# Kernel tuning notes

Hardware: AMD Instinct MI355X
Metric: run time of the kernel (lower is better)

The kernel has to match this reference:

```python
import jax, jax.numpy as jnp
import numpy as np

# Dimensions (see shape_source)
B, C, H, W = 8, 3, 256, 256
WIDTH = 32   # FNO width
MODES = 12   # modes1 == modes2
L = 4        # number of FNO layers
GAP = 4      # encoder_de sample_gap
PAD = 9      # trans_net.padding


def _downsample(x):
    # Faithful vectorized form of encoder_de.output: keep indices i % GAP == 0
    # (output size int((N-1)/GAP)+1 == number of multiples of GAP below N).
    return x[:, :, ::GAP, ::GAP]


def _spectral_conv(x, w1, w2):
    # SpectralConv2d: rfft2 -> low-mode complex channel mix -> irfft2
    Hp, Wp = x.shape[-2], x.shape[-1]
    x_ft = jnp.fft.rfft2(x)  # [B, WIDTH, Hp, Wp//2+1] complex64
    out_ft = jnp.zeros((x.shape[0], w1.shape[1], Hp, Wp // 2 + 1), dtype=jnp.complex64)
    out_ft = out_ft.at[:, :, :MODES, :MODES].set(
        jnp.einsum('bixy,ioxy->boxy', x_ft[:, :, :MODES, :MODES], w1))
    out_ft = out_ft.at[:, :, -MODES:, :MODES].set(
        jnp.einsum('bixy,ioxy->boxy', x_ft[:, :, -MODES:, :MODES], w2))
    return jnp.fft.irfft2(out_ft, s=(Hp, Wp))


def _forward(x_en, fc0_w, fc0_b, w1r, w1i, w2r, w2i, pw_w, pw_b,
             fc1_w, fc1_b, fc2_w, fc2_b):
    x_de = _downsample(x_en)
    # fc0 on channels-last, back to channels-first
    x = jnp.einsum('bchw,cd->bdhw', x_en, fc0_w) + fc0_b[None, :, None, None]
    # F.pad(x, [0, PAD, 0, PAD]) pads right/bottom of last two dims
    x = jnp.pad(x, ((0, 0), (0, 0), (0, PAD), (0, PAD)))
    for l in range(L):
        w1 = (w1r[l] + 1j * w1i[l]).astype(jnp.complex64)
        w2 = (w2r[l] + 1j * w2i[l]).astype(jnp.complex64)
        x1 = _spectral_conv(x, w1, w2)
        x2 = jnp.einsum('bihw,oi->bohw', x, pw_w[l]) + pw_b[l][None, :, None, None]
        x = x1 + x2
        if l < L - 1:  # last layer has no activation
            x = jax.nn.gelu(x, approximate=False)  # torch F.gelu default = exact erf
    trans_out = x[..., :-PAD, :-PAD].transpose(0, 2, 3, 1)  # [B,H,W,WIDTH]
    h = jax.nn.gelu(trans_out @ fc1_w + fc1_b, approximate=False)  # [B,H,W,128]
    pred_delta = (h @ fc2_w + fc2_b).transpose(0, 3, 1, 2)          # [B,3,H,W]
    pred = pred_delta + x_en
    pred_de = _downsample(pred)
    return pred_de, x_de, pred, x_en


def setup_inputs() -> dict:
    key = jax.random.key(0)
    ks = jax.random.split(key, 14)
    scale = 1.0 / (WIDTH * WIDTH)
    f32 = jnp.float32
    x_en = jax.random.normal(ks[0], (B, C, H, W), f32)
    ctr = jnp.zeros((B, 1), f32)  # accepted but unused by trans_net.forward
    fc0_w = jax.random.normal(ks[1], (3, WIDTH), f32) * 0.2
    fc0_b = jnp.zeros((WIDTH,), f32)
    # torch.rand(..., dtype=cfloat): uniform [0,1) real and imag parts
    w1r = scale * jax.random.uniform(ks[2], (L, WIDTH, WIDTH, MODES, MODES), f32)
    w1i = scale * jax.random.uniform(ks[3], (L, WIDTH, WIDTH, MODES, MODES), f32)
    w2r = scale * jax.random.uniform(ks[4], (L, WIDTH, WIDTH, MODES, MODES), f32)
    w2i = scale * jax.random.uniform(ks[5], (L, WIDTH, WIDTH, MODES, MODES), f32)
    pw_w = jax.random.normal(ks[6], (L, WIDTH, WIDTH), f32) / np.sqrt(WIDTH)  # 1x1 conv [out,in]
    pw_b = jnp.zeros((L, WIDTH), f32)
    fc1_w = jax.random.normal(ks[7], (WIDTH, 128), f32) / np.sqrt(WIDTH)
    fc1_b = jnp.zeros((128,), f32)
    fc2_w = jax.random.normal(ks[8], (128, 3), f32) / np.sqrt(128.0)
    fc2_b = jnp.zeros((3,), f32)
    return dict(x_en=x_en, ctr=ctr, fc0_w=fc0_w, fc0_b=fc0_b,
                w1r=w1r, w1i=w1i, w2r=w2r, w2i=w2i,
                pw_w=pw_w, pw_b=pw_b, fc1_w=fc1_w, fc1_b=fc1_b,
                fc2_w=fc2_w, fc2_b=fc2_b)


def reference(x_en, ctr, fc0_w, fc0_b, w1r, w1i, w2r, w2i, pw_w, pw_b,
              fc1_w, fc1_b, fc2_w, fc2_b):
    del ctr  # unused in the original trans_net.forward
    return _forward(x_en, fc0_w, fc0_b, w1r, w1i, w2r, w2i, pw_w, pw_b,
                    fc1_w, fc1_b, fc2_w, fc2_b)
```

## Files before the change

kernel.cpp:

```cpp
#include <hip/hip_runtime.h>
#include <math.h>

#define HP 265
#define NPIX 70225
#define ROWF 8480
#define TWO_PI 6.28318530717958647692f

#define OFF_X     0
#define OFF_U     8988800
#define OFF_G     10752640
#define OFF_A     11047552
#define OFF_TFB   12132992
#define OFF_TS    12137600
#define OFF_W1B   12141952
#define OFF_W2B   12144000
#define OFF_PWB   12145024

typedef __attribute__((ext_vector_type(8))) short short8;
typedef __attribute__((ext_vector_type(4))) float f32x4;

__device__ __forceinline__ float gelu_f(float v){
  float x2 = v*v;
  float p  = fmaf(x2, 0.10295597f, 2.30212056f);
  float tn = -v*p;
  float e  = __builtin_amdgcn_exp2f(tn);
  float r  = __builtin_amdgcn_rcpf(1.0f + e);
  return v * r;
}
__device__ __forceinline__ unsigned short f2b(float f){
  unsigned u = __float_as_uint(f);
  u += 0x7FFFu + ((u >> 16) & 1u);
  return (unsigned short)(u >> 16);
}
__device__ __forceinline__ unsigned pk(unsigned short lo, unsigned short hi){
  return (unsigned)lo | ((unsigned)hi << 16);
}

__global__ void k_init(unsigned short* __restrict__ Tfb, unsigned short* __restrict__ Ts,
                       unsigned short* __restrict__ w1b, unsigned short* __restrict__ w2b,
                       unsigned short* __restrict__ pwb,
                       const float* __restrict__ fc1w, const float* __restrict__ fc2w,
                       const float* __restrict__ pw_w){
  int idx = blockIdx.x*256 + threadIdx.x;
  if (idx < 32*288){
    int m = idx / 288, hc = idx % 288;
    unsigned short v = 0;
    if (m < 26 && hc < 265){
      int k = m >> 1;
      int t = (hc*k) % HP;
      float s, c; sincosf(TWO_PI*(float)t/(float)HP, &s, &c);
      v = f2b((m & 1) ? -s : c);
    }
    Tfb[idx] = v;
  }
  if (idx < 272*32){
    int w = idx >> 5, kap = idx & 31;
    unsigned short v = 0;
    if (w < HP && kap < 24){
      int k = kap >> 1;
      int t = (w*k) % HP;
      float s, c; sincosf(TWO_PI*(float)t/(float)HP, &s, &c);
      const float invN = 1.f/70225.f;
      float val = (!(kap&1)) ? invN*(k==0 ? 1.f : 2.f*c)
                             : ((k==0) ? 0.f : -invN*2.f*s);
      v = f2b(val);
    }
    Ts[idx] = v;
  }
  if (idx < 4096){
    int n = idx >> 5, k = idx & 31;
    w1b[idx] = f2b(fc1w[k*128 + n]);
  }
  if (idx < 2048){
    int n = idx >> 7, k = idx & 127;
    w2b[idx] = (n < 3) ? f2b(fc2w[k*3 + n]) : (unsigned short)0;
  }
  if (idx < 4096)
    pwb[idx] = f2b(pw_w[idx]);
}

__global__ __launch_bounds__(256) void k_fc0(const float* __restrict__ xen,
                                             const float* __restrict__ w0,
                                             const float* __restrict__ b0,
                                             unsigned short* __restrict__ xb,
                                             float* __restrict__ out){
  int idx = blockIdx.x*256 + threadIdx.x;
  if (idx >= 8*NPIX) return;
  int w = idx % HP; int t = idx / HP; int h = t % HP; int b = t / HP;
  unsigned short o16[32];
  if (h < 256 && w < 256){
    const float* xp = xen + (((size_t)b*3)*256 + h)*256 + w;
    float c0 = xp[0], c1 = xp[65536], c2 = xp[131072];
    #pragma unroll
    for (int d = 0; d < 32; ++d)
      o16[d] = f2b(b0[d] + c0*w0[d] + c1*w0[32+d] + c2*w0[64+d]);
    size_t be = ((size_t)b*3)*65536 + (h<<8) + w;
    out[1769472 + be]          = c0;
    out[1769472 + be + 65536]  = c1;
    out[1769472 + be + 131072] = c2;
    if (((h|w)&3) == 0){
      size_t db = ((size_t)b*3)*4096 + ((h>>2)<<6) + (w>>2);
      out[98304 + db]        = c0;
      out[98304 + db + 4096] = c1;
      out[98304 + db + 8192] = c2;
    }
  } else {
    #pragma unroll
    for (int d = 0; d < 32; ++d) o16[d] = 0;
  }
  uint4* dst = (uint4*)(xb + (size_t)idx*32);
  #pragma unroll
  for (int q = 0; q < 4; ++q)
    dst[q] = make_uint4(pk(o16[8*q],o16[8*q+1]), pk(o16[8*q+2],o16[8*q+3]),
                        pk(o16[8*q+4],o16[8*q+5]), pk(o16[8*q+6],o16[8*q+7]));
}

__global__ __launch_bounds__(256) void k_dftm(const unsigned short* __restrict__ xb,
                                              const unsigned short* __restrict__ Tfb,
                                              float* __restrict__ U32){
  int tid = threadIdx.x;
  int wv = tid>>6, lane = tid&63, lr = lane&15, g = lane>>4, lk = g*8;
  int n0 = blockIdx.x*64;
  int b  = blockIdx.y;
  int n  = n0 + wv*16 + lr;
  const unsigned short* xcol = xb + (size_t)b*HP*ROWF + n;
  f32x4 acc0 = {0.f,0.f,0.f,0.f}, acc1 = {0.f,0.f,0.f,0.f};
  #pragma unroll
  for (int kc = 0; kc < 9; ++kc){
    short8 hv;
    int hb = kc*32 + lk;
    #pragma unroll
    for (int q = 0; q < 8; ++q){
      int h = hb + q;
      hv[q] = (h < HP) ? (short)xcol[(size_t)h*ROWF] : (short)0;
    }
    short8 aT0 = *(const short8*)&Tfb[lr*288 + kc*32 + lk];
    short8 aT1 = *(const short8*)&Tfb[(16+lr)*288 + kc*32 + lk];
    acc0 = __builtin_amdgcn_mfma_f32_16x16x32_bf16(aT0, hv, acc0, 0,0,0);
    acc1 = __builtin_amdgcn_mfma_f32_16x16x32_bf16(aT1, hv, acc1, 0,0,0);
  }
  if (n < 8480){
    #pragma unroll
    for (int r = 0; r < 4; ++r){
      int m0 = g*4 + r;
      U32[((size_t)b*26 + m0)*8480 + n] = acc0[r];
      int m1 = 16 + m0;
      if (m1 < 26) U32[((size_t)b*26 + m1)*8480 + n] = acc1[r];
    }
  }
}

__global__ __launch_bounds__(256) void k_spec(const float* __restrict__ U32,
                                              const float* __restrict__ w1r,
                                              const float* __restrict__ w1i,
                                              const float* __restrict__ w2r,
                                              const float* __restrict__ w2i,
                                              float2* __restrict__ G, int l){
  __shared__ float part[256*25];
  __shared__ float Xs[32*25];
  int j = blockIdx.x;
  int b = blockIdx.y;
  int ws = blockIdx.z;
  int tid = threadIdx.x;
  int wsub = tid >> 5, i = tid & 31;
  int kk   = (j < 12) ? j : (24 - j);
  bool cj  = (j >= 12);
  float xr[12], xi[12];
  #pragma unroll
  for (int k = 0; k < 12; ++k){ xr[k] = 0.f; xi[k] = 0.f; }
  const float* ubr = U32 + ((size_t)(b*26 + 2*kk))*8480;
  for (int w = ws*8 + wsub; w < HP; w += 16){
    int n = w*32 + i;
    float ux = ubr[n];
    float uy = ubr[8480 + n];
    if (cj) uy = -uy;
    float bs, bc; sincosf(-TWO_PI*(float)w/(float)HP, &bs, &bc);
    float pr = 1.f, pi = 0.f;
    #pragma unroll
    for (int k = 0; k < 12; ++k){
      xr[k] = fmaf(ux, pr, fmaf(-uy, pi, xr[k]));
      xi[k] = fmaf(ux, pi, fmaf( uy, pr, xi[k]));
      float npr = pr*bc - pi*bs;
      pi = fmaf(pr, bs, pi*bc);
      pr = npr;
    }
  }
  #pragma unroll
  for (int k = 0; k < 12; ++k){
    part[tid*25 + 2*k]     = xr[k];
    part[tid*25 + 2*k + 1] = xi[k];
  }
  __syncthreads();
  {
    int sg = tid >> 5;
    int ii = tid & 31;
    #pragma unroll
    for (int s0 = 0; s0 < 3; ++s0){
      int s = sg*3 + s0;
      float acc = 0.f;
      #pragma unroll
      for (int wq = 0; wq < 8; ++wq) acc += part[(wq*32 + ii)*25 + s];
      Xs[ii*25 + s] = acc;
    }
  }
  __syncthreads();
  int ky = (j < 12) ? j : (j - 12);
  const float* wr = (j < 12) ? w1r : w2r;
  const float* wi = (j < 12) ? w1i : w2i;
  float2* Gp = G + (size_t)ws*73728;
  for (int p = tid; p < 384; p += 256){
    int o = p / 12, kx = p % 12;
    size_t wbase = (size_t)l*147456 + (size_t)o*144 + (size_t)ky*12 + kx;
    float gr = 0.f, gi = 0.f;
    #pragma unroll 4
    for (int i2 = 0; i2 < 32; ++i2){
      float xvr = Xs[i2*25 + 2*kx];
      float xvi = Xs[i2*25 + 2*kx + 1];
      float a = wr[wbase + (size_t)i2*4608];
      float c = wi[wbase + (size_t)i2*4608];
      gr += xvr*a - xvi*c;
      gi += xvr*c + xvi*a;
    }
    Gp[((size_t)(b*32 + o)*24 + j)*12 + kx] = make_float2(gr, gi);
  }
}

__global__ __launch_bounds__(320) void k_idft_h(const float2* __restrict__ G,
                                                unsigned short* __restrict__ A16){
  __shared__ float2 gs[288];
  int bo = blockIdx.x;
  for (int i = threadIdx.x; i < 288; i += 320){
    float2 g0 = G[(size_t)bo*288 + i];
    float2 g1 = G[73728 + (size_t)bo*288 + i];
    gs[i] = make_float2(g0.x + g1.x, g0.y + g1.y);
  }
  __syncthreads();
  int h = threadIdx.x;
  if (h >= HP) return;
  float ar[12], ai[12];
  #pragma unroll
  for (int k = 0; k < 12; ++k){ ar[k] = 0.f; ai[k] = 0.f; }
  for (int j = 0; j < 24; ++j){
    int ky = (j < 12) ? j : (241 + j);
    int t = (ky*h) % HP;
    float s, c; sincosf(TWO_PI*(float)t/(float)HP, &s, &c);
    #pragma unroll
    for (int k = 0; k < 12; ++k){
      float2 g = gs[j*12 + k];
      ar[k] = fmaf(g.x, c, fmaf(-g.y, s, ar[k]));
      ai[k] = fmaf(g.x, s, fmaf( g.y, c, ai[k]));
    }
  }
  int b = bo >> 5, o = bo & 31;
  unsigned short o16[32];
  #pragma unroll
  for (int k = 0; k < 12; ++k){ o16[2*k] = f2b(ar[k]); o16[2*k+1] = f2b(ai[k]); }
  #pragma unroll
  for (int k = 24; k < 32; ++k) o16[k] = 0;
  uint4* ap = (uint4*)(A16 + (((size_t)(b*HP + h))*32 + o)*32);
  #pragma unroll
  for (int q = 0; q < 4; ++q)
    ap[q] = make_uint4(pk(o16[8*q],o16[8*q+1]), pk(o16[8*q+2],o16[8*q+3]),
                       pk(o16[8*q+4],o16[8*q+5]), pk(o16[8*q+6],o16[8*q+7]));
}

__global__ __launch_bounds__(256) void k_final(const unsigned short* __restrict__ A16,
                                               const unsigned short* __restrict__ Tsyn,
                                               const unsigned short* __restrict__ pwb,
                                               const float* __restrict__ pw_b,
                                               unsigned short* __restrict__ xb, int l){
  int tid = threadIdx.x;
  int wv = tid>>6, lane = tid&63, lr = lane&15, g = lane>>4, lk = g*8;
  int h = blockIdx.x*4 + wv;
  int b = blockIdx.y;
  if (h >= HP) return;
  const unsigned short* arow = A16 + (size_t)(b*HP + h)*1024;
  short8 aA0 = *(const short8*)&arow[lr*32 + lk];
  short8 aA1 = *(const short8*)&arow[(16+lr)*32 + lk];
  short8 aP0 = *(const short8*)&pwb[l*1024 + lr*32 + lk];
  short8 aP1 = *(const short8*)&pwb[l*1024 + (16+lr)*32 + lk];
  float4 vb0 = *(const float4*)&pw_b[l*32 + g*4];
  float4 vb1 = *(const float4*)&pw_b[l*32 + 16 + g*4];
  unsigned short* xrow = xb + (size_t)(b*HP + h)*ROWF;
  const f32x4 z4 = {0.f,0.f,0.f,0.f};
  for (int wt = 0; wt < 17; ++wt){
    int w = wt*16 + lr;
    short8 bT = *(const short8*)&Tsyn[(size_t)w*32 + lk];
    short8 bX = *(const short8*)&xrow[(size_t)w*32 + lk];
    f32x4 a0 = __builtin_amdgcn_mfma_f32_16x16x32_bf16(aA0, bT, z4, 0,0,0);
    a0 = __builtin_amdgcn_mfma_f32_16x16x32_bf16(aP0, bX, a0, 0,0,0);
    f32x4 a1 = __builtin_amdgcn_mfma_f32_16x16x32_bf16(aA1, bT, z4, 0,0,0);
    a1 = __builtin_amdgcn_mfma_f32_16x16x32_bf16(aP1, bX, a1, 0,0,0);
    if (w < HP){
      float v0[4], v1[4];
      v0[0]=a0[0]+vb0.x; v0[1]=a0[1]+vb0.y; v0[2]=a0[2]+vb0.z; v0[3]=a0[3]+vb0.w;
      v1[0]=a1[0]+vb1.x; v1[1]=a1[1]+vb1.y; v1[2]=a1[2]+vb1.z; v1[3]=a1[3]+vb1.w;
      if (l < 3){
        #pragma unroll
        for (int r = 0; r < 4; ++r){ v0[r] = gelu_f(v0[r]); v1[r] = gelu_f(v1[r]); }
      }
      *(uint2*)&xrow[(size_t)w*32 + g*4] =
          make_uint2(pk(f2b(v0[0]),f2b(v0[1])), pk(f2b(v0[2]),f2b(v0[3])));
      *(uint2*)&xrow[(size_t)w*32 + 16 + g*4] =
          make_uint2(pk(f2b(v1[0]),f2b(v1[1])), pk(f2b(v1[2]),f2b(v1[3])));
    }
  }
}

__global__ __launch_bounds__(256) void k_head(const unsigned short* __restrict__ xb,
                                              const float* __restrict__ xen,
                                              const unsigned short* __restrict__ w1b,
                                              const float* __restrict__ fc1b,
                                              const unsigned short* __restrict__ w2b,
                                              const float* __restrict__ fc2b,
                                              float* __restrict__ out){
  __shared__ unsigned short Pm[4][16*136];
  int tid = threadIdx.x;
  int b = blockIdx.x >> 8, h = blockIdx.x & 255;
  int wv = tid>>6, lane = tid&63, lr = lane&15, g = lane>>4, lk = g*8;
  short8 bf1[8], bf2[4];
  #pragma unroll
  for (int nt = 0; nt < 8; ++nt)
    bf1[nt] = *(const short8*)&w1b[(nt*16+lr)*32 + lk];
  #pragma unroll
  for (int ks = 0; ks < 4; ++ks)
    bf2[ks] = *(const short8*)&w2b[lr*128 + ks*32 + lk];
  float f2c = (lr < 3) ? fc2b[lr] : 0.f;
  const unsigned short* xrow = xb + (size_t)(b*HP + h)*ROWF;
  unsigned short* P = Pm[wv];
  const f32x4 z4 = {0.f,0.f,0.f,0.f};
  #pragma unroll
  for (int m = 0; m < 4; ++m){
    int p0 = (wv*4 + m)*16;
    short8 ax = *(const short8*)&xrow[(size_t)(p0 + lr)*32 + lk];
    f32x4 acc[8];
    #pragma unroll
    for (int nt = 0; nt < 8; ++nt)
      acc[nt] = __builtin_amdgcn_mfma_f32_16x16x32_bf16(bf1[nt], ax, z4, 0,0,0);
    #pragma unroll
    for (int nt = 0; nt < 8; ++nt){
      float4 bb = *(const float4*)&fc1b[nt*16 + g*4];
      float h0 = gelu_f(acc[nt][0] + bb.x);
      float h1 = gelu_f(acc[nt][1] + bb.y);
      float h2 = gelu_f(acc[nt][2] + bb.z);
      float h3 = gelu_f(acc[nt][3] + bb.w);
      *(uint2*)&P[lr*136 + nt*16 + g*4] =
          make_uint2(pk(f2b(h0),f2b(h1)), pk(f2b(h2),f2b(h3)));
    }
    asm volatile("s_waitcnt lgkmcnt(0)" ::: "memory");
    __builtin_amdgcn_sched_barrier(0);
    f32x4 a2 = z4;
    #pragma unroll
    for (int ks = 0; ks < 4; ++ks){
      short8 ap = *(const short8*)&P[lr*136 + ks*32 + lk];
      a2 = __builtin_amdgcn_mfma_f32_16x16x32_bf16(ap, bf2[ks], a2, 0,0,0);
    }
    if (lr < 3){
      size_t base = ((size_t)(b*3 + lr))*65536 + (h<<8) + p0 + g*4;
      float4 xe = *(const float4*)&xen[base];
      float4 pr;
      pr.x = a2[0] + f2c + xe.x;
      pr.y = a2[1] + f2c + xe.y;
      pr.z = a2[2] + f2c + xe.z;
      pr.w = a2[3] + f2c + xe.w;
      *(float4*)&out[196608 + base] = pr;
      if ((h & 3) == 0){
        int w4 = (p0 + g*4) >> 2;
        out[((size_t)(b*3 + lr))*4096 + ((h>>2)<<6) + w4] = pr.x;
      }
    }
  }
}

extern "C" void kernel_launch(void* const* d_in, const int* in_sizes, int n_in,
                              void* d_out, int out_size, void* d_ws, size_t ws_size,
                              hipStream_t stream){
  const float* x_en  = (const float*)d_in[0];
  const float* fc0_w = (const float*)d_in[2];
  const float* fc0_b = (const float*)d_in[3];
  const float* w1r   = (const float*)d_in[4];
  const float* w1i   = (const float*)d_in[5];
  const float* w2r   = (const float*)d_in[6];
  const float* w2i   = (const float*)d_in[7];
  const float* pw_w  = (const float*)d_in[8];
  const float* pw_b  = (const float*)d_in[9];
  const float* fc1_w = (const float*)d_in[10];
  const float* fc1_b = (const float*)d_in[11];
  const float* fc2_w = (const float*)d_in[12];
  const float* fc2_b = (const float*)d_in[13];
  float* out = (float*)d_out;
  float* ws  = (float*)d_ws;

  unsigned short* xb  = (unsigned short*)(ws + OFF_X);
  float*  U32         = ws + OFF_U;
  float2* G           = (float2*)(ws + OFF_G);
  unsigned short* A16 = (unsigned short*)(ws + OFF_A);
  unsigned short* Tfb = (unsigned short*)(ws + OFF_TFB);
  unsigned short* Ts  = (unsigned short*)(ws + OFF_TS);
  unsigned short* w1b = (unsigned short*)(ws + OFF_W1B);
  unsigned short* w2b = (unsigned short*)(ws + OFF_W2B);
  unsigned short* pwb = (unsigned short*)(ws + OFF_PWB);

  k_init<<<36, 256, 0, stream>>>(Tfb, Ts, w1b, w2b, pwb, fc1_w, fc2_w, pw_w);
  k_fc0<<<2195, 256, 0, stream>>>(x_en, fc0_w, fc0_b, xb, out);
  for (int l = 0; l < 4; ++l){
    k_dftm<<<dim3(133,8), 256, 0, stream>>>(xb, Tfb, U32);
    k_spec<<<dim3(24,8,2), 256, 0, stream>>>(U32, w1r, w1i, w2r, w2i, G, l);
    k_idft_h<<<256, 320, 0, stream>>>(G, A16);
    k_final<<<dim3(67,8), 256, 0, stream>>>(A16, Ts, pwb, pw_b, xb, l);
  }
  k_head<<<2048, 256, 0, stream>>>(xb, x_en, w1b, fc1_b, w2b, fc2_b, out);
}
```

Before: 323.3 us.

## Fuse init into fc0, widen spec/final grids, double-buffer head LDS stage

Folds the one-time table/weight conversion into the fc0 kernel as extra blocks, removing a launch. Splits the spectral-mix W reduction four ways instead of two and sums four partials in the inverse DFT, and splits k_final's width tiles across two z-blocks to raise occupancy. In the head kernel the fc1/fc2 stages are software-pipelined with a double-buffered shared tile so the fc2 of one chunk overlaps the fc1 of the next. Costs are more partial-sum traffic, a larger workspace layout, and more shared memory per block.

```diff
diff --git a/kernel.cpp b/kernel.cpp
--- a/kernel.cpp
+++ b/kernel.cpp
@@ -9,12 +9,12 @@
 #define OFF_X     0
 #define OFF_U     8988800
 #define OFF_G     10752640
-#define OFF_A     11047552
-#define OFF_TFB   12132992
-#define OFF_TS    12137600
-#define OFF_W1B   12141952
-#define OFF_W2B   12144000
-#define OFF_PWB   12145024
+#define OFF_A     11342464
+#define OFF_TFB   12427904
+#define OFF_TS    12432512
+#define OFF_W1B   12436864
+#define OFF_W2B   12438912
+#define OFF_PWB   12439936
 
 typedef __attribute__((ext_vector_type(8))) short short8;
 typedef __attribute__((ext_vector_type(4))) float f32x4;
@@ -36,12 +36,12 @@
   return (unsigned)lo | ((unsigned)hi << 16);
 }
 
-__global__ void k_init(unsigned short* __restrict__ Tfb, unsigned short* __restrict__ Ts,
+__device__ __forceinline__ void init_body(int idx,
+                       unsigned short* __restrict__ Tfb, unsigned short* __restrict__ Ts,
                        unsigned short* __restrict__ w1b, unsigned short* __restrict__ w2b,
                        unsigned short* __restrict__ pwb,
                        const float* __restrict__ fc1w, const float* __restrict__ fc2w,
                        const float* __restrict__ pw_w){
-  int idx = blockIdx.x*256 + threadIdx.x;
   if (idx < 32*288){
     int m = idx / 288, hc = idx % 288;
     unsigned short v = 0;
@@ -83,7 +83,20 @@
                                              const float* __restrict__ w0,
                                              const float* __restrict__ b0,
                                              unsigned short* __restrict__ xb,
-                                             float* __restrict__ out){
+                                             float* __restrict__ out,
+                                             unsigned short* __restrict__ Tfb,
+                                             unsigned short* __restrict__ Ts,
+                                             unsigned short* __restrict__ w1b,
+                                             unsigned short* __restrict__ w2b,
+                                             unsigned short* __restrict__ pwb,
+                                             const float* __restrict__ fc1w,
+                                             const float* __restrict__ fc2w,
+                                             const float* __restrict__ pw_w){
+  if (blockIdx.x >= 2195){
+    init_body((blockIdx.x - 2195)*256 + threadIdx.x, Tfb, Ts, w1b, w2b, pwb,
+              fc1w, fc2w, pw_w);
+    return;
+  }
   int idx = blockIdx.x*256 + threadIdx.x;
   if (idx >= 8*NPIX) return;
   int w = idx % HP; int t = idx / HP; int h = t % HP; int b = t / HP;
@@ -169,7 +182,7 @@
   #pragma unroll
   for (int k = 0; k < 12; ++k){ xr[k] = 0.f; xi[k] = 0.f; }
   const float* ubr = U32 + ((size_t)(b*26 + 2*kk))*8480;
-  for (int w = ws*8 + wsub; w < HP; w += 16){
+  for (int w = ws*8 + wsub; w < HP; w += 32){
     int n = w*32 + i;
     float ux = ubr[n];
     float uy = ubr[8480 + n];
@@ -232,7 +245,9 @@
   for (int i = threadIdx.x; i < 288; i += 320){
     float2 g0 = G[(size_t)bo*288 + i];
     float2 g1 = G[73728 + (size_t)bo*288 + i];
-    gs[i] = make_float2(g0.x + g1.x, g0.y + g1.y);
+    float2 g2 = G[2*73728 + (size_t)bo*288 + i];
+    float2 g3 = G[3*73728 + (size_t)bo*288 + i];
+    gs[i] = make_float2(g0.x+g1.x+g2.x+g3.x, g0.y+g1.y+g2.y+g3.y);
   }
   __syncthreads();
   int h = threadIdx.x;
@@ -273,6 +288,7 @@
   int wv = tid>>6, lane = tid&63, lr = lane&15, g = lane>>4, lk = g*8;
   int h = blockIdx.x*4 + wv;
   int b = blockIdx.y;
+  int z = blockIdx.z;
   if (h >= HP) return;
   const unsigned short* arow = A16 + (size_t)(b*HP + h)*1024;
   short8 aA0 = *(const short8*)&arow[lr*32 + lk];
@@ -283,7 +299,8 @@
   float4 vb1 = *(const float4*)&pw_b[l*32 + 16 + g*4];
   unsigned short* xrow = xb + (size_t)(b*HP + h)*ROWF;
   const f32x4 z4 = {0.f,0.f,0.f,0.f};
-  for (int wt = 0; wt < 17; ++wt){
+  int wt0 = z ? 9 : 0, wt1 = z ? 17 : 9;
+  for (int wt = wt0; wt < wt1; ++wt){
     int w = wt*16 + lr;
     short8 bT = *(const short8*)&Tsyn[(size_t)w*32 + lk];
     short8 bX = *(const short8*)&xrow[(size_t)w*32 + lk];
@@ -314,7 +331,7 @@
                                               const unsigned short* __restrict__ w2b,
                                               const float* __restrict__ fc2b,
                                               float* __restrict__ out){
-  __shared__ unsigned short Pm[4][16*136];
+  __shared__ unsigned short Pm[4][2][16*136];
   int tid = threadIdx.x;
   int b = blockIdx.x >> 8, h = blockIdx.x & 255;
   int wv = tid>>6, lane = tid&63, lr = lane&15, g = lane>>4, lk = g*8;
@@ -327,16 +344,16 @@
     bf2[ks] = *(const short8*)&w2b[lr*128 + ks*32 + lk];
   float f2c = (lr < 3) ? fc2b[lr] : 0.f;
   const unsigned short* xrow = xb + (size_t)(b*HP + h)*ROWF;
-  unsigned short* P = Pm[wv];
   const f32x4 z4 = {0.f,0.f,0.f,0.f};
-  #pragma unroll
-  for (int m = 0; m < 4; ++m){
+
+  auto STAGE = [&](int m){
     int p0 = (wv*4 + m)*16;
     short8 ax = *(const short8*)&xrow[(size_t)(p0 + lr)*32 + lk];
     f32x4 acc[8];
     #pragma unroll
     for (int nt = 0; nt < 8; ++nt)
       acc[nt] = __builtin_amdgcn_mfma_f32_16x16x32_bf16(bf1[nt], ax, z4, 0,0,0);
+    unsigned short* P = Pm[wv][m & 1];
     #pragma unroll
     for (int nt = 0; nt < 8; ++nt){
       float4 bb = *(const float4*)&fc1b[nt*16 + g*4];
@@ -347,8 +364,9 @@
       *(uint2*)&P[lr*136 + nt*16 + g*4] =
           make_uint2(pk(f2b(h0),f2b(h1)), pk(f2b(h2),f2b(h3)));
     }
-    asm volatile("s_waitcnt lgkmcnt(0)" ::: "memory");
-    __builtin_amdgcn_sched_barrier(0);
+  };
+  auto FC2 = [&](int m){
+    const unsigned short* P = Pm[wv][m & 1];
     f32x4 a2 = z4;
     #pragma unroll
     for (int ks = 0; ks < 4; ++ks){
@@ -356,6 +374,7 @@
       a2 = __builtin_amdgcn_mfma_f32_16x16x32_bf16(ap, bf2[ks], a2, 0,0,0);
     }
     if (lr < 3){
+      int p0 = (wv*4 + m)*16;
       size_t base = ((size_t)(b*3 + lr))*65536 + (h<<8) + p0 + g*4;
       float4 xe = *(const float4*)&xen[base];
       float4 pr;
@@ -369,7 +388,17 @@
         out[((size_t)(b*3 + lr))*4096 + ((h>>2)<<6) + w4] = pr.x;
       }
     }
-  }
+  };
+
+  STAGE(0);
+  asm volatile("s_waitcnt lgkmcnt(0)" ::: "memory");
+  #pragma unroll
+  for (int m = 1; m < 4; ++m){
+    STAGE(m);
+    FC2(m - 1);
+    asm volatile("s_waitcnt lgkmcnt(0)" ::: "memory");
+  }
+  FC2(3);
 }
 
 extern "C" void kernel_launch(void* const* d_in, const int* in_sizes, int n_in,
@@ -401,13 +430,13 @@
   unsigned short* w2b = (unsigned short*)(ws + OFF_W2B);
   unsigned short* pwb = (unsigned short*)(ws + OFF_PWB);
 
-  k_init<<<36, 256, 0, stream>>>(Tfb, Ts, w1b, w2b, pwb, fc1_w, fc2_w, pw_w);
-  k_fc0<<<2195, 256, 0, stream>>>(x_en, fc0_w, fc0_b, xb, out);
+  k_fc0<<<2231, 256, 0, stream>>>(x_en, fc0_w, fc0_b, xb, out,
+                                  Tfb, Ts, w1b, w2b, pwb, fc1_w, fc2_w, pw_w);
   for (int l = 0; l < 4; ++l){
     k_dftm<<<dim3(133,8), 256, 0, stream>>>(xb, Tfb, U32);
-    k_spec<<<dim3(24,8,2), 256, 0, stream>>>(U32, w1r, w1i, w2r, w2i, G, l);
+    k_spec<<<dim3(24,8,4), 256, 0, stream>>>(U32, w1r, w1i, w2r, w2i, G, l);
     k_idft_h<<<256, 320, 0, stream>>>(G, A16);
-    k_final<<<dim3(67,8), 256, 0, stream>>>(A16, Ts, pwb, pw_b, xb, l);
+    k_final<<<dim3(67,8,2), 256, 0, stream>>>(A16, Ts, pwb, pw_b, xb, l);
   }
   k_head<<<2048, 256, 0, stream>>>(xb, x_en, w1b, fc1_b, w2b, fc2_b, out);
 }
```

After: 303.3 us. 1.07x faster.
